# Kernel optimization log

Measured on AMD Instinct MI355X. Metric: run time of the kernel, lower is better.

The kernel has to match this reference:

```python
import jax, jax.numpy as jnp
import numpy as np

H = 512      # hidden_size
GH = 512     # global_hidden_size
V = 128      # VOCAB_SIZE (one-hot arg_hot width)
D = 14       # tree depth; complete binary tree
NUM_OPS = 36
N_INT = 5    # num_internal_ops
N_NODES = 2 ** (D + 1) - 1  # 32767, heap layout: node i has children 2i+1, 2i+2


def _p(key, i, shape, s=0.05):
    return jax.random.normal(jax.random.fold_in(key, i), shape, dtype=jnp.float32) * s


def setup_inputs() -> dict:
    key = jax.random.key(0)
    return {
        "tokens": jax.random.randint(jax.random.fold_in(key, 0), (N_NODES,), 0, V),
        "validity_mask": jnp.ones((NUM_OPS,), jnp.float32),
        # binary tree-LSTM (blstm): 2 children
        "W_iou_b": _p(key, 1, (V, 3 * H)), "U_iou_b": _p(key, 2, (2, H, 3 * H)), "b_iou_b": jnp.zeros((3 * H,), jnp.float32),
        "Wf_b": _p(key, 3, (V, H)), "Uf_b": _p(key, 4, (2, H, H)), "bf_b": jnp.ones((H,), jnp.float32),
        # ternary tree-LSTM (tlstm): 3 children
        "W_iou_t": _p(key, 5, (V, 3 * H)), "U_iou_t": _p(key, 6, (3, H, 3 * H)), "b_iou_t": jnp.zeros((3 * H,), jnp.float32),
        "Wf_t": _p(key, 7, (V, H)), "Uf_t": _p(key, 8, (3, H, H)), "bf_t": jnp.ones((H,), jnp.float32),
        # FFN: one h-by-h layer (ffn_complexity = h^2 * n_layers, n_layers=1)
        "ffn_W": _p(key, 9, (H, H)), "ffn_b": jnp.zeros((H,), jnp.float32),
        # global LSTM (1 layer, 1 step), torch gate order i,f,g,o
        "lstm_Wx": _p(key, 10, (H, 4 * GH)), "lstm_Wh": _p(key, 11, (GH, 4 * GH)), "lstm_b": jnp.zeros((4 * GH,), jnp.float32),
        # actor heads on concat(root_hidden, h_glob)
        "hl_W": _p(key, 12, (H + GH, 2)), "hl_b": jnp.zeros((2,), jnp.float32),
        "int_W": _p(key, 13, (H + GH, N_INT)), "int_b": jnp.zeros((N_INT,), jnp.float32),
        "act_W": _p(key, 14, (H + GH, NUM_OPS)), "act_b": jnp.zeros((NUM_OPS,), jnp.float32),
    }


def _nary_cell(x, hk, ck, W_iou, U_iou, b_iou, Wf, Uf, bf):
    # x: [n, V]; hk, ck: [n, K, H]  (K children)
    iou = x @ W_iou + jnp.einsum('nkh,khg->ng', hk, U_iou) + b_iou
    i, o, u = jnp.split(iou, 3, axis=-1)
    f = jax.nn.sigmoid((x @ Wf + bf)[:, None, :] + jnp.einsum('nkh,khg->nkg', hk, Uf))
    c = jax.nn.sigmoid(i) * jnp.tanh(u) + jnp.sum(f * ck, axis=1)
    h = jax.nn.sigmoid(o) * jnp.tanh(c)
    return h, c


def _forward(tokens, validity_mask, W_iou_b, U_iou_b, b_iou_b, Wf_b, Uf_b, bf_b,
             W_iou_t, U_iou_t, b_iou_t, Wf_t, Uf_t, bf_t, ffn_W, ffn_b,
             lstm_Wx, lstm_Wh, lstm_b, hl_W, hl_b, int_W, int_b, act_W, act_b):
    arg_hot = jax.nn.one_hot(tokens, V, dtype=jnp.float32)  # [N_NODES, V]
    h_prev = c_prev = None
    h_ab = c_ab = None
    # apply_binary_lstm over the whole tree, bottom-up, one batched cell per level
    for lvl in range(D, -1, -1):
        n = 2 ** lvl
        x = arg_hot[n - 1:2 * n - 1]  # level lvl occupies heap slots [2^l-1, 2^{l+1}-2]
        if h_prev is None:
            hk = jnp.zeros((n, 2, H), jnp.float32)  # leaves: tz children
            ck = hk
        else:
            hk = h_prev.reshape(n, 2, H)
            ck = c_prev.reshape(n, 2, H)
        h_prev, c_prev = _nary_cell(x, hk, ck, W_iou_b, U_iou_b, b_iou_b, Wf_b, Uf_b, bf_b)
        if lvl == 1:
            h_ab, c_ab = h_prev, c_prev  # root's children a, b
    # apply_ternary_lstm at depth 0: children = (self.hidden, a.hidden, b.hidden)
    hk3 = jnp.concatenate([h_prev, h_ab], axis=0)[None]  # [1, 3, H]
    ck3 = jnp.concatenate([c_prev, c_ab], axis=0)[None]
    h_root, c_root = _nary_cell(arg_hot[0:1], hk3, ck3, W_iou_t, U_iou_t, b_iou_t, Wf_t, Uf_t, bf_t)
    # apply_ffn (1 layer) then apply_global_lstm (single step from zero state)
    h_f = jnp.maximum(h_root @ ffn_W + ffn_b, 0.0)  # [1, H]
    h_g = jnp.zeros((1, GH), jnp.float32)
    c_g = h_g
    gates = h_f @ lstm_Wx + h_g @ lstm_Wh + lstm_b
    gi, gf, gg, go = jnp.split(gates, 4, axis=-1)
    c_g = jax.nn.sigmoid(gf) * c_g + jax.nn.sigmoid(gi) * jnp.tanh(gg)
    h_g = jax.nn.sigmoid(go) * jnp.tanh(c_g)
    # actor heads
    feat = jnp.concatenate([h_f, h_g], axis=-1)  # [1, H+GH]
    hl = feat @ hl_W + hl_b
    il = feat @ int_W + int_b
    el = jnp.log(validity_mask)[None, :] + feat @ (act_W * validity_mask[None, :]) + act_b * validity_mask
    return jnp.concatenate([hl, il, el], axis=-1)  # [1, 2 + N_INT + NUM_OPS]


def reference(tokens, validity_mask, W_iou_b, U_iou_b, b_iou_b, Wf_b, Uf_b, bf_b,
              W_iou_t, U_iou_t, b_iou_t, Wf_t, Uf_t, bf_t, ffn_W, ffn_b,
              lstm_Wx, lstm_Wh, lstm_b, hl_W, hl_b, int_W, int_b, act_W, act_b):
    return _forward(tokens, validity_mask, W_iou_b, U_iou_b, b_iou_b, Wf_b, Uf_b, bf_b,
                    W_iou_t, U_iou_t, b_iou_t, Wf_t, Uf_t, bf_t, ffn_W, ffn_b,
                    lstm_Wx, lstm_Wh, lstm_b, hl_W, hl_b, int_W, int_b, act_W, act_b)
```

## Files before the change

### kernel.cpp

```cpp
#include <hip/hip_runtime.h>
#include <hip/hip_bf16.h>
#include <math.h>

#define H 512
#define V 128
#define NLEAF 16384

typedef __attribute__((ext_vector_type(4))) float f32x4;
typedef __attribute__((ext_vector_type(8))) short s16x8;
typedef unsigned short ushort_t;

__device__ ushort_t g_hb0[NLEAF * H];
__device__ ushort_t g_hb1[(NLEAF / 2) * H];
__device__ float    g_c0[NLEAF * H];
__device__ float    g_c1[(NLEAF / 2) * H];
__device__ ushort_t g_UiouT[3 * H * 2 * H];
__device__ ushort_t g_UfT[H * 2 * H];
__device__ ushort_t g_UiouTt[3 * H * 3 * H];
__device__ ushort_t g_UfTt[H * 3 * H];
__device__ float    g_rpart[3 * 3072];
__device__ float    g_spart[32 * 2 * 2560];
__device__ float    g_root[2 * H];
__device__ float    g_hf[H];
__device__ float    g_gates[4 * H];

__device__ __forceinline__ float sigm(float x) { return 1.0f / (1.0f + __expf(-x)); }
__device__ __forceinline__ float ftanh(float x) {
  return 1.0f - 2.0f / (__expf(2.0f * x) + 1.0f);
}
__device__ __forceinline__ ushort_t f2bf(float x) {
  __hip_bfloat16 b = __float2bfloat16(x);
  return *reinterpret_cast<ushort_t*>(&b);
}
__device__ __forceinline__ float bf2f(ushort_t u) {
  union { unsigned int i; float f; } v; v.i = ((unsigned int)u) << 16; return v.f;
}
__device__ __forceinline__ void gload_lds16(const void* g, void* l) {
  __builtin_amdgcn_global_load_lds(
      (const __attribute__((address_space(1))) unsigned int*)g,
      (__attribute__((address_space(3))) unsigned int*)l, 16, 0, 0);
}

__global__ __launch_bounds__(256) void k_transp(const float* __restrict__ src,
                                                ushort_t* __restrict__ dst,
                                                int R, int Cc) {
  __shared__ float t[32][33];
  int bc = blockIdx.x * 32, br = blockIdx.y * 32;
  int tx = threadIdx.x & 31, ty = threadIdx.x >> 5;
  for (int rr = ty; rr < 32; rr += 8)
    t[rr][tx] = src[(size_t)(br + rr) * Cc + bc + tx];
  __syncthreads();
  for (int rr = ty; rr < 32; rr += 8)
    dst[(size_t)(bc + rr) * R + br + tx] = f2bf(t[tx][rr]);
}

__global__ __launch_bounds__(256) void k_leaf(const int* __restrict__ tokens,
                                              const float* __restrict__ Wiou,
                                              const float* __restrict__ biou) {
  int idx = blockIdx.x * 256 + threadIdx.x;
  int i = idx >> 9, j = idx & (H - 1);
  int tok = tokens[(NLEAF - 1) + i];
  const float* Wr = Wiou + (size_t)tok * 3 * H;
  float ig = Wr[j] + biou[j];
  float og = Wr[H + j] + biou[H + j];
  float ug = Wr[2 * H + j] + biou[2 * H + j];
  float c = sigm(ig) * ftanh(ug);
  float h = sigm(og) * ftanh(c);
  g_hb0[idx] = f2bf(h);
  g_c0[idx] = c;
}

__global__ __launch_bounds__(256, 2) void k_mfma_lvl(int lvl,
    const int* __restrict__ tokens,
    const float* __restrict__ Wiou, const float* __restrict__ biou,
    const float* __restrict__ Wf, const float* __restrict__ bf) {
  const int n = 1 << lvl;
  const int node0 = n - 1;
  const int outp = lvl & 1;
  const ushort_t* __restrict__ hprev = outp ? g_hb0 : g_hb1;
  const float* __restrict__ cprev = outp ? g_c0 : g_c1;
  ushort_t* __restrict__ hout = outp ? g_hb1 : g_hb0;
  float* __restrict__ cout = outp ? g_c1 : g_c0;

  const int i0 = blockIdx.x * 128;
  const int j0 = blockIdx.y * 64;
  const int tid = threadIdx.x;
  const int lane = tid & 63;
  const int w = tid >> 6;
  const int wry = w >> 1;
  const int cx = w & 1;

  __shared__ f32x4 smemv[3072];
  char* smem = (char*)smemv;

  const char* gp[6];
  unsigned lb[6], lstride[6];
  {
    int kb = (lane >> 4) * 16;
    #pragma unroll
    for (int q = 0; q < 6; ++q) {
      int c = w * 6 + q;
      if (c < 8) {
        int row = i0 + c * 16 + (lane & 15);
        gp[q] = (const char*)hprev + (size_t)row * 2048 + kb;
        lb[q] = c * 1024u;
        lstride[q] = 8192u;
      } else {
        int ct = c - 8;
        int col = ct * 16 + (lane & 15);
        int g = col >> 6, jj = j0 + (col & 63);
        const ushort_t* Ub = (g < 3) ? (g_UiouT + (size_t)(g * 512 + jj) * 1024)
                                     : (g_UfT + (size_t)jj * 1024);
        gp[q] = (const char*)Ub + kb;
        lb[q] = 16384u + ct * 1024u;
        lstride[q] = 16384u;
      }
    }
  }

#define STAGE(BUF)                                                   \
  {                                                                  \
    _Pragma("unroll")                                                \
    for (int q = 0; q < 6; ++q) {                                    \
      gload_lds16(gp[q], smem + lb[q] + (unsigned)(BUF) * lstride[q]); \
      gp[q] += 64;                                                   \
    }                                                                \
  }

  f32x4 acc[4][10];
  #pragma unroll
  for (int a = 0; a < 4; ++a)
    #pragma unroll
    for (int b = 0; b < 10; ++b) acc[a][b] = (f32x4){0.f, 0.f, 0.f, 0.f};

#define COMPUTE(FA)                                                          \
  {                                                                          \
    const char* ab = smem + buf * 8192 + wry * 4096 + lane * 16;             \
    s16x8 a0 = *(const s16x8*)(ab);                                          \
    s16x8 a1 = *(const s16x8*)(ab + 1024);                                   \
    s16x8 a2 = *(const s16x8*)(ab + 2048);                                   \
    s16x8 a3 = *(const s16x8*)(ab + 3072);                                   \
    const char* bb = smem + 16384 + buf * 16384 + cx * 2048 + lane * 16;     \
    s16x8 b0 = *(const s16x8*)(bb);                                          \
    s16x8 b1 = *(const s16x8*)(bb + 1024);                                   \
    s16x8 b2 = *(const s16x8*)(bb + 4096);                                   \
    s16x8 b3 = *(const s16x8*)(bb + 5120);                                   \
    s16x8 b4 = *(const s16x8*)(bb + 8192);                                   \
    s16x8 b5 = *(const s16x8*)(bb + 9216);                                   \
    s16x8 b6 = *(const s16x8*)(bb + 12288);                                  \
    s16x8 b7 = *(const s16x8*)(bb + 13312);                                  \
    s16x8 aa[4] = {a0, a1, a2, a3};                                          \
    _Pragma("unroll")                                                        \
    for (int rtl = 0; rtl < 4; ++rtl) {                                      \
      acc[rtl][0] = __builtin_amdgcn_mfma_f32_16x16x32_bf16(aa[rtl], b0, acc[rtl][0], 0, 0, 0); \
      acc[rtl][1] = __builtin_amdgcn_mfma_f32_16x16x32_bf16(aa[rtl], b1, acc[rtl][1], 0, 0, 0); \
      acc[rtl][2] = __builtin_amdgcn_mfma_f32_16x16x32_bf16(aa[rtl], b2, acc[rtl][2], 0, 0, 0); \
      acc[rtl][3] = __builtin_amdgcn_mfma_f32_16x16x32_bf16(aa[rtl], b3, acc[rtl][3], 0, 0, 0); \
      acc[rtl][4] = __builtin_amdgcn_mfma_f32_16x16x32_bf16(aa[rtl], b4, acc[rtl][4], 0, 0, 0); \
      acc[rtl][5] = __builtin_amdgcn_mfma_f32_16x16x32_bf16(aa[rtl], b5, acc[rtl][5], 0, 0, 0); \
      acc[rtl][FA] = __builtin_amdgcn_mfma_f32_16x16x32_bf16(aa[rtl], b6, acc[rtl][FA], 0, 0, 0); \
      acc[rtl][FA + 1] = __builtin_amdgcn_mfma_f32_16x16x32_bf16(aa[rtl], b7, acc[rtl][FA + 1], 0, 0, 0); \
    }                                                                        \
  }

  STAGE(0);
  __syncthreads();
  int buf = 0;
  for (int kt = 0; kt < 16; ++kt) {
    STAGE(buf ^ 1);
    COMPUTE(6);
    __syncthreads();
    buf ^= 1;
  }
  for (int kt = 16; kt < 32; ++kt) {
    if (kt < 31) STAGE(buf ^ 1);
    COMPUTE(8);
    __syncthreads();
    buf ^= 1;
  }
#undef COMPUTE
#undef STAGE

  const int node_c = lane >> 4;
  const int jl = lane & 15;
  #pragma unroll
  for (int t = 0; t < 2; ++t) {
    const int j = j0 + cx * 32 + t * 16 + jl;
    const float bi = biou[j], bo = biou[512 + j], bu = biou[1024 + j], bfv = bf[j];
    #pragma unroll
    for (int rtl = 0; rtl < 4; ++rtl) {
      f32x4 vi = acc[rtl][0 + t], vo = acc[rtl][2 + t], vu = acc[rtl][4 + t],
            v0 = acc[rtl][6 + t], v1 = acc[rtl][8 + t];
      const int ib = i0 + wry * 64 + rtl * 16 + node_c * 4;
      #pragma unroll
      for (int r = 0; r < 4; ++r) {
        int i = ib + r;
        if (i < n) {
          int tok = tokens[node0 + i];
          const float* Wr = Wiou + (size_t)tok * 1536;
          float fpre = Wf[(size_t)tok * 512 + j] + bfv;
          float ig = vi[r] + Wr[j] + bi;
          float og = vo[r] + Wr[512 + j] + bo;
          float ug = vu[r] + Wr[1024 + j] + bu;
          float cc = sigm(ig) * ftanh(ug)
                   + sigm(fpre + v0[r]) * cprev[(size_t)(2 * i) * 512 + j]
                   + sigm(fpre + v1[r]) * cprev[(size_t)(2 * i + 1) * 512 + j];
          float hh = sigm(og) * ftanh(cc);
          hout[(size_t)i * 512 + j] = f2bf(hh);
          cout[(size_t)i * 512 + j] = cc;
        }
      }
    }
  }
}

__global__ __launch_bounds__(256) void k_sm_p1(int lvl) {
  const int outp = lvl & 1;
  const ushort_t* __restrict__ hprev = outp ? g_hb0 : g_hb1;
  const int i = blockIdx.z;
  const int by = blockIdx.y;
  const int tid = threadIdx.x;
  const int c = blockIdx.x * 256 + tid;

  __shared__ float hl[512];
  hl[tid] = bf2f(hprev[(size_t)i * 1024 + by * 512 + tid]);
  hl[256 + tid] = bf2f(hprev[(size_t)i * 1024 + by * 512 + 256 + tid]);
  __syncthreads();

  float acc = 0.f;
  const ushort_t* col = nullptr;
  if (c < 1536) {
    col = g_UiouT + (size_t)c * 1024 + by * 512;
  } else {
    int v = c - 1536;
    if ((v >> 9) == by) col = g_UfT + (size_t)(v & 511) * 1024 + by * 512;
  }
  if (col) {
    #pragma unroll 4
    for (int k0 = 0; k0 < 512; k0 += 8) {
      s16x8 wv = *(const s16x8*)(col + k0);
      #pragma unroll
      for (int r = 0; r < 8; ++r) acc += hl[k0 + r] * bf2f((ushort_t)wv[r]);
    }
  }
  g_spart[((size_t)i * 2 + by) * 2560 + c] = acc;
}

__global__ __launch_bounds__(512) void k_sm_p2(int lvl,
    const int* __restrict__ tokens,
    const float* __restrict__ Wiou, const float* __restrict__ biou,
    const float* __restrict__ Wf, const float* __restrict__ bf) {
  const int n = 1 << lvl;
  const int node0 = n - 1;
  const int outp = lvl & 1;
  const float* __restrict__ cprev = outp ? g_c0 : g_c1;
  ushort_t* __restrict__ hout = outp ? g_hb1 : g_hb0;
  float* __restrict__ cout = outp ? g_c1 : g_c0;

  const int i = blockIdx.x;
  const int j = threadIdx.x;
  const float* sp = g_spart + (size_t)i * 2 * 2560;

  float ai = sp[j] + sp[2560 + j];
  float ao = sp[512 + j] + sp[2560 + 512 + j];
  float au = sp[1024 + j] + sp[2560 + 1024 + j];
  float af0 = sp[1536 + j] + sp[2560 + 1536 + j];
  float af1 = sp[2048 + j] + sp[2560 + 2048 + j];

  int tok = tokens[node0 + i];
  const float* Wr = Wiou + (size_t)tok * 1536;
  float fpre = Wf[(size_t)tok * 512 + j] + bf[j];
  float ig = ai + Wr[j] + biou[j];
  float og = ao + Wr[512 + j] + biou[512 + j];
  float ug = au + Wr[1024 + j] + biou[1024 + j];
  float cc = sigm(ig) * ftanh(ug)
           + sigm(fpre + af0) * cprev[(size_t)(2 * i) * 512 + j]
           + sigm(fpre + af1) * cprev[(size_t)(2 * i + 1) * 512 + j];
  float hh = sigm(og) * ftanh(cc);
  hout[(size_t)i * 512 + j] = f2bf(hh);
  cout[(size_t)i * 512 + j] = cc;
}

__global__ __launch_bounds__(256) void k_root_p1() {
  const int by = blockIdx.y;
  const int tid = threadIdx.x;
  const int c = blockIdx.x * 256 + tid;

  __shared__ float hl[512];
  {
    int m0 = by * 512;
    #pragma unroll
    for (int q = 0; q < 2; ++q) {
      int t = tid + q * 256, m = m0 + t;
      hl[t] = (m < 512) ? bf2f(g_hb0[m]) : bf2f(g_hb1[m - 512]);
    }
  }
  __syncthreads();

  float acc = 0.f;
  const ushort_t* col = nullptr;
  if (c < 1536) {
    col = g_UiouTt + (size_t)c * 1536 + by * 512;
  } else {
    int v = c - 1536;
    if ((v >> 9) == by) col = g_UfTt + (size_t)(v & 511) * 1536 + by * 512;
  }
  if (col) {
    #pragma unroll 4
    for (int k0 = 0; k0 < 512; k0 += 8) {
      s16x8 wv = *(const s16x8*)(col + k0);
      #pragma unroll
      for (int r = 0; r < 8; ++r) acc += hl[k0 + r] * bf2f((ushort_t)wv[r]);
    }
  }
  g_rpart[(size_t)by * 3072 + c] = acc;
}

__global__ __launch_bounds__(512) void k_root_p2(const int* __restrict__ tokens,
    const float* __restrict__ Wiou_t, const float* __restrict__ biou_t,
    const float* __restrict__ Wf_t, const float* __restrict__ bf_t) {
  const int j = threadIdx.x;
  float ai = g_rpart[j] + g_rpart[3072 + j] + g_rpart[6144 + j];
  float ao = g_rpart[512 + j] + g_rpart[3072 + 512 + j] + g_rpart[6144 + 512 + j];
  float au = g_rpart[1024 + j] + g_rpart[3072 + 1024 + j] + g_rpart[6144 + 1024 + j];
  float f0 = g_rpart[1536 + j] + g_rpart[3072 + 1536 + j] + g_rpart[6144 + 1536 + j];
  float f1 = g_rpart[2048 + j] + g_rpart[3072 + 2048 + j] + g_rpart[6144 + 2048 + j];
  float f2 = g_rpart[2560 + j] + g_rpart[3072 + 2560 + j] + g_rpart[6144 + 2560 + j];

  int tok = tokens[0];
  float fpre = Wf_t[(size_t)tok * H + j] + bf_t[j];
  float ig = ai + Wiou_t[(size_t)tok * 3 * H + j] + biou_t[j];
  float og = ao + Wiou_t[(size_t)tok * 3 * H + H + j] + biou_t[H + j];
  float ug = au + Wiou_t[(size_t)tok * 3 * H + 2 * H + j] + biou_t[2 * H + j];
  float cc = sigm(ig) * ftanh(ug)
           + sigm(fpre + f0) * g_c0[j]
           + sigm(fpre + f1) * g_c1[j]
           + sigm(fpre + f2) * g_c1[H + j];
  float hh = sigm(og) * ftanh(cc);
  g_root[j] = hh;
  g_root[H + j] = cc;
}

__global__ __launch_bounds__(512) void k_head1(const float* __restrict__ ffnW,
                                               const float* __restrict__ ffnb) {
  __shared__ float hr[H];
  int j = threadIdx.x;
  hr[j] = g_root[j];
  __syncthreads();
  float acc = ffnb[j];
  #pragma unroll 8
  for (int m = 0; m < H; ++m) acc += hr[m] * ffnW[m * H + j];
  g_hf[j] = fmaxf(acc, 0.0f);
}

__global__ __launch_bounds__(64) void k_head2(const float* __restrict__ Wx,
                                              const float* __restrict__ lb) {
  int g = blockIdx.x * 64 + threadIdx.x;
  float acc = lb[g];
  #pragma unroll 8
  for (int m = 0; m < H; ++m) acc += g_hf[m] * Wx[m * 4 * H + g];
  g_gates[g] = acc;
}

__global__ __launch_bounds__(512) void k_head3(const float* __restrict__ vm,
    const float* __restrict__ hlW, const float* __restrict__ hlb,
    const float* __restrict__ intW, const float* __restrict__ intb,
    const float* __restrict__ actW, const float* __restrict__ actb,
    float* __restrict__ out) {
  __shared__ float feat[2 * H];
  int j = threadIdx.x;
  float ci = sigm(g_gates[j]) * ftanh(g_gates[2 * H + j]);
  float hg = sigm(g_gates[3 * H + j]) * ftanh(ci);
  feat[j] = g_hf[j];
  feat[H + j] = hg;
  __syncthreads();

  const int wv = threadIdx.x >> 6;
  const int lane = threadIdx.x & 63;
  for (int o = wv; o < 43; o += 8) {
    const float* Wc;
    int stride, colb;
    if (o < 2)       { Wc = hlW;  stride = 2;  colb = o; }
    else if (o < 7)  { Wc = intW; stride = 5;  colb = o - 2; }
    else             { Wc = actW; stride = 36; colb = o - 7; }
    float s = 0.f;
    #pragma unroll
    for (int q = 0; q < 16; ++q) {
      int m = lane + q * 64;
      s += feat[m] * Wc[(size_t)m * stride + colb];
    }
    #pragma unroll
    for (int d = 32; d >= 1; d >>= 1) s += __shfl_xor(s, d);
    if (lane == 0) {
      float res;
      if (o < 2)      res = s + hlb[o];
      else if (o < 7) res = s + intb[o - 2];
      else {
        int a = o - 7;
        float v = vm[a];
        res = __logf(v) + s * v + actb[a] * v;
      }
      out[o] = res;
    }
  }
}

extern "C" void kernel_launch(void* const* d_in, const int* in_sizes, int n_in,
                              void* d_out, int out_size, void* d_ws, size_t ws_size,
                              hipStream_t stream) {
  (void)in_sizes; (void)n_in; (void)d_ws; (void)ws_size; (void)out_size;
  const int* tokens   = (const int*)d_in[0];
  const float* vm     = (const float*)d_in[1];
  const float* Wiou_b = (const float*)d_in[2];
  const float* Uiou_b = (const float*)d_in[3];
  const float* biou_b = (const float*)d_in[4];
  const float* Wf_b   = (const float*)d_in[5];
  const float* Uf_b   = (const float*)d_in[6];
  const float* bf_b   = (const float*)d_in[7];
  const float* Wiou_t = (const float*)d_in[8];
  const float* Uiou_t = (const float*)d_in[9];
  const float* biou_t = (const float*)d_in[10];
  const float* Wf_t   = (const float*)d_in[11];
  const float* Uf_t   = (const float*)d_in[12];
  const float* bf_t   = (const float*)d_in[13];
  const float* ffnW   = (const float*)d_in[14];
  const float* ffnb   = (const float*)d_in[15];
  const float* lstmWx = (const float*)d_in[16];
  const float* lstmb  = (const float*)d_in[18];
  const float* hlW    = (const float*)d_in[19];
  const float* hlb    = (const float*)d_in[20];
  const float* intW   = (const float*)d_in[21];
  const float* intb   = (const float*)d_in[22];
  const float* actW   = (const float*)d_in[23];
  const float* actb   = (const float*)d_in[24];

  ushort_t* UiouT;  hipGetSymbolAddress((void**)&UiouT, HIP_SYMBOL(g_UiouT));
  ushort_t* UfT;    hipGetSymbolAddress((void**)&UfT, HIP_SYMBOL(g_UfT));
  ushort_t* UiouTt; hipGetSymbolAddress((void**)&UiouTt, HIP_SYMBOL(g_UiouTt));
  ushort_t* UfTt;   hipGetSymbolAddress((void**)&UfTt, HIP_SYMBOL(g_UfTt));

  k_transp<<<dim3(48, 32), 256, 0, stream>>>(Uiou_b, UiouT, 1024, 1536);
  k_transp<<<dim3(16, 32), 256, 0, stream>>>(Uf_b, UfT, 1024, 512);
  k_transp<<<dim3(48, 48), 256, 0, stream>>>(Uiou_t, UiouTt, 1536, 1536);
  k_transp<<<dim3(16, 48), 256, 0, stream>>>(Uf_t, UfTt, 1536, 512);

  k_leaf<<<NLEAF * H / 256, 256, 0, stream>>>(tokens, Wiou_b, biou_b);
  for (int lvl = 13; lvl >= 6; --lvl) {
    int gx = (1 << lvl) / 128; if (gx < 1) gx = 1;
    k_mfma_lvl<<<dim3(gx, 8), 256, 0, stream>>>(lvl, tokens, Wiou_b, biou_b,
                                                Wf_b, bf_b);
  }
  for (int lvl = 5; lvl >= 0; --lvl) {
    int n = 1 << lvl;
    k_sm_p1<<<dim3(10, 2, n), 256, 0, stream>>>(lvl);
    k_sm_p2<<<n, 512, 0, stream>>>(lvl, tokens, Wiou_b, biou_b, Wf_b, bf_b);
  }
  k_root_p1<<<dim3(12, 3), 256, 0, stream>>>();
  k_root_p2<<<1, 512, 0, stream>>>(tokens, Wiou_t, biou_t, Wf_t, bf_t);
  k_head1<<<1, 512, 0, stream>>>(ffnW, ffnb);
  k_head2<<<32, 64, 0, stream>>>(lstmWx, lstmb);
  k_head3<<<1, 512, 0, stream>>>(vm, hlW, hlb, intW, intb, actW, actb, (float*)d_out);
}
```

Before: 671.9 us.

## Shrink MFMA level tiles, vectorize leaf kernel, fuse small-level GEMV passes

The MFMA level kernel drops from 128-row tiles with 4 waves to 64-row tiles with 2 waves, each wave covering all 64 rows and 32 columns. This doubles block count on the mid-size levels to fill more CUs, at the cost of less B-tile reuse per block. The leaf kernel becomes a grid-stride loop with float4 loads and vector stores. The two-kernel small-level path (partial sums plus combine) is merged into one kernel that reduces in shared memory, removing a launch and the global partial buffer per level.

```diff
diff --git a/kernel.cpp b/kernel.cpp
--- a/kernel.cpp
+++ b/kernel.cpp
@@ -8,6 +8,7 @@
 
 typedef __attribute__((ext_vector_type(4))) float f32x4;
 typedef __attribute__((ext_vector_type(8))) short s16x8;
+typedef __attribute__((ext_vector_type(4))) unsigned short u16x4;
 typedef unsigned short ushort_t;
 
 __device__ ushort_t g_hb0[NLEAF * H];
@@ -19,7 +20,6 @@
 __device__ ushort_t g_UiouTt[3 * H * 3 * H];
 __device__ ushort_t g_UfTt[H * 3 * H];
 __device__ float    g_rpart[3 * 3072];
-__device__ float    g_spart[32 * 2 * 2560];
 __device__ float    g_root[2 * H];
 __device__ float    g_hf[H];
 __device__ float    g_gates[4 * H];
@@ -57,20 +57,29 @@
 __global__ __launch_bounds__(256) void k_leaf(const int* __restrict__ tokens,
                                               const float* __restrict__ Wiou,
                                               const float* __restrict__ biou) {
-  int idx = blockIdx.x * 256 + threadIdx.x;
-  int i = idx >> 9, j = idx & (H - 1);
-  int tok = tokens[(NLEAF - 1) + i];
-  const float* Wr = Wiou + (size_t)tok * 3 * H;
-  float ig = Wr[j] + biou[j];
-  float og = Wr[H + j] + biou[H + j];
-  float ug = Wr[2 * H + j] + biou[2 * H + j];
-  float c = sigm(ig) * ftanh(ug);
-  float h = sigm(og) * ftanh(c);
-  g_hb0[idx] = f2bf(h);
-  g_c0[idx] = c;
-}
-
-__global__ __launch_bounds__(256, 2) void k_mfma_lvl(int lvl,
+  const int total = NLEAF * 128;
+  for (int q = blockIdx.x * 256 + threadIdx.x; q < total; q += gridDim.x * 256) {
+    int i = q >> 7, jv = q & 127;
+    int tok = tokens[(NLEAF - 1) + i];
+    const f32x4* Wr = (const f32x4*)(Wiou + (size_t)tok * 1536);
+    const f32x4* bv = (const f32x4*)biou;
+    f32x4 wi = Wr[jv] + bv[jv];
+    f32x4 wo = Wr[128 + jv] + bv[128 + jv];
+    f32x4 wu = Wr[256 + jv] + bv[256 + jv];
+    u16x4 hv; f32x4 cv;
+    #pragma unroll
+    for (int r = 0; r < 4; ++r) {
+      float c = sigm(wi[r]) * ftanh(wu[r]);
+      float h = sigm(wo[r]) * ftanh(c);
+      cv[r] = c;
+      hv[r] = f2bf(h);
+    }
+    *reinterpret_cast<u16x4*>(&g_hb0[(size_t)q * 4]) = hv;
+    *reinterpret_cast<f32x4*>(&g_c0[(size_t)q * 4]) = cv;
+  }
+}
+
+__global__ __launch_bounds__(128, 2) void k_mfma_lvl(int lvl,
     const int* __restrict__ tokens,
     const float* __restrict__ Wiou, const float* __restrict__ biou,
     const float* __restrict__ Wf, const float* __restrict__ bf) {
@@ -82,49 +91,47 @@
   ushort_t* __restrict__ hout = outp ? g_hb1 : g_hb0;
   float* __restrict__ cout = outp ? g_c1 : g_c0;
 
-  const int i0 = blockIdx.x * 128;
+  const int i0 = blockIdx.x * 64;
   const int j0 = blockIdx.y * 64;
   const int tid = threadIdx.x;
   const int lane = tid & 63;
   const int w = tid >> 6;
-  const int wry = w >> 1;
-  const int cx = w & 1;
-
-  __shared__ f32x4 smemv[3072];
+
+  __shared__ f32x4 smemv[2560];
   char* smem = (char*)smemv;
 
-  const char* gp[6];
-  unsigned lb[6], lstride[6];
+  const char* gp[10];
+  unsigned lb[10], lstr[10];
   {
     int kb = (lane >> 4) * 16;
     #pragma unroll
-    for (int q = 0; q < 6; ++q) {
-      int c = w * 6 + q;
-      if (c < 8) {
+    for (int q = 0; q < 10; ++q) {
+      int c = w * 10 + q;
+      if (c < 4) {
         int row = i0 + c * 16 + (lane & 15);
         gp[q] = (const char*)hprev + (size_t)row * 2048 + kb;
         lb[q] = c * 1024u;
-        lstride[q] = 8192u;
+        lstr[q] = 4096u;
       } else {
-        int ct = c - 8;
+        int ct = c - 4;
         int col = ct * 16 + (lane & 15);
         int g = col >> 6, jj = j0 + (col & 63);
         const ushort_t* Ub = (g < 3) ? (g_UiouT + (size_t)(g * 512 + jj) * 1024)
                                      : (g_UfT + (size_t)jj * 1024);
         gp[q] = (const char*)Ub + kb;
-        lb[q] = 16384u + ct * 1024u;
-        lstride[q] = 16384u;
+        lb[q] = 8192u + ct * 1024u;
+        lstr[q] = 16384u;
       }
     }
   }
 
-#define STAGE(BUF)                                                   \
-  {                                                                  \
-    _Pragma("unroll")                                                \
-    for (int q = 0; q < 6; ++q) {                                    \
-      gload_lds16(gp[q], smem + lb[q] + (unsigned)(BUF) * lstride[q]); \
-      gp[q] += 64;                                                   \
-    }                                                                \
+#define STAGE(BUF)                                                     \
+  {                                                                    \
+    _Pragma("unroll")                                                  \
+    for (int q = 0; q < 10; ++q) {                                     \
+      gload_lds16(gp[q], smem + lb[q] + (unsigned)(BUF) * lstr[q]);    \
+      gp[q] += 64;                                                     \
+    }                                                                  \
   }
 
   f32x4 acc[4][10];
@@ -135,12 +142,12 @@
 
 #define COMPUTE(FA)                                                          \
   {                                                                          \
-    const char* ab = smem + buf * 8192 + wry * 4096 + lane * 16;             \
+    const char* ab = smem + buf * 4096 + lane * 16;                          \
     s16x8 a0 = *(const s16x8*)(ab);                                          \
     s16x8 a1 = *(const s16x8*)(ab + 1024);                                   \
     s16x8 a2 = *(const s16x8*)(ab + 2048);                                   \
     s16x8 a3 = *(const s16x8*)(ab + 3072);                                   \
-    const char* bb = smem + 16384 + buf * 16384 + cx * 2048 + lane * 16;     \
+    const char* bb = smem + 8192 + buf * 16384 + w * 2048 + lane * 16;       \
     s16x8 b0 = *(const s16x8*)(bb);                                          \
     s16x8 b1 = *(const s16x8*)(bb + 1024);                                   \
     s16x8 b2 = *(const s16x8*)(bb + 4096);                                   \
@@ -185,100 +192,93 @@
   const int jl = lane & 15;
   #pragma unroll
   for (int t = 0; t < 2; ++t) {
-    const int j = j0 + cx * 32 + t * 16 + jl;
+    const int j = j0 + w * 32 + t * 16 + jl;
     const float bi = biou[j], bo = biou[512 + j], bu = biou[1024 + j], bfv = bf[j];
     #pragma unroll
     for (int rtl = 0; rtl < 4; ++rtl) {
       f32x4 vi = acc[rtl][0 + t], vo = acc[rtl][2 + t], vu = acc[rtl][4 + t],
             v0 = acc[rtl][6 + t], v1 = acc[rtl][8 + t];
-      const int ib = i0 + wry * 64 + rtl * 16 + node_c * 4;
+      const int ib = i0 + rtl * 16 + node_c * 4;
       #pragma unroll
       for (int r = 0; r < 4; ++r) {
         int i = ib + r;
-        if (i < n) {
-          int tok = tokens[node0 + i];
-          const float* Wr = Wiou + (size_t)tok * 1536;
-          float fpre = Wf[(size_t)tok * 512 + j] + bfv;
-          float ig = vi[r] + Wr[j] + bi;
-          float og = vo[r] + Wr[512 + j] + bo;
-          float ug = vu[r] + Wr[1024 + j] + bu;
-          float cc = sigm(ig) * ftanh(ug)
-                   + sigm(fpre + v0[r]) * cprev[(size_t)(2 * i) * 512 + j]
-                   + sigm(fpre + v1[r]) * cprev[(size_t)(2 * i + 1) * 512 + j];
-          float hh = sigm(og) * ftanh(cc);
-          hout[(size_t)i * 512 + j] = f2bf(hh);
-          cout[(size_t)i * 512 + j] = cc;
-        }
+        int tok = tokens[node0 + i];
+        const float* Wr = Wiou + (size_t)tok * 1536;
+        float fpre = Wf[(size_t)tok * 512 + j] + bfv;
+        float ig = vi[r] + Wr[j] + bi;
+        float og = vo[r] + Wr[512 + j] + bo;
+        float ug = vu[r] + Wr[1024 + j] + bu;
+        float cc = sigm(ig) * ftanh(ug)
+                 + sigm(fpre + v0[r]) * cprev[(size_t)(2 * i) * 512 + j]
+                 + sigm(fpre + v1[r]) * cprev[(size_t)(2 * i + 1) * 512 + j];
+        float hh = sigm(og) * ftanh(cc);
+        hout[(size_t)i * 512 + j] = f2bf(hh);
+        cout[(size_t)i * 512 + j] = cc;
       }
     }
   }
 }
 
-__global__ __launch_bounds__(256) void k_sm_p1(int lvl) {
-  const int outp = lvl & 1;
-  const ushort_t* __restrict__ hprev = outp ? g_hb0 : g_hb1;
-  const int i = blockIdx.z;
-  const int by = blockIdx.y;
-  const int tid = threadIdx.x;
-  const int c = blockIdx.x * 256 + tid;
-
-  __shared__ float hl[512];
-  hl[tid] = bf2f(hprev[(size_t)i * 1024 + by * 512 + tid]);
-  hl[256 + tid] = bf2f(hprev[(size_t)i * 1024 + by * 512 + 256 + tid]);
-  __syncthreads();
-
-  float acc = 0.f;
-  const ushort_t* col = nullptr;
-  if (c < 1536) {
-    col = g_UiouT + (size_t)c * 1024 + by * 512;
-  } else {
-    int v = c - 1536;
-    if ((v >> 9) == by) col = g_UfT + (size_t)(v & 511) * 1024 + by * 512;
-  }
-  if (col) {
-    #pragma unroll 4
-    for (int k0 = 0; k0 < 512; k0 += 8) {
-      s16x8 wv = *(const s16x8*)(col + k0);
-      #pragma unroll
-      for (int r = 0; r < 8; ++r) acc += hl[k0 + r] * bf2f((ushort_t)wv[r]);
-    }
-  }
-  g_spart[((size_t)i * 2 + by) * 2560 + c] = acc;
-}
-
-__global__ __launch_bounds__(512) void k_sm_p2(int lvl,
+__global__ __launch_bounds__(256) void k_small(int lvl,
     const int* __restrict__ tokens,
     const float* __restrict__ Wiou, const float* __restrict__ biou,
     const float* __restrict__ Wf, const float* __restrict__ bf) {
   const int n = 1 << lvl;
   const int node0 = n - 1;
   const int outp = lvl & 1;
+  const ushort_t* __restrict__ hprev = outp ? g_hb0 : g_hb1;
   const float* __restrict__ cprev = outp ? g_c0 : g_c1;
   ushort_t* __restrict__ hout = outp ? g_hb1 : g_hb0;
   float* __restrict__ cout = outp ? g_c1 : g_c0;
 
-  const int i = blockIdx.x;
-  const int j = threadIdx.x;
-  const float* sp = g_spart + (size_t)i * 2 * 2560;
-
-  float ai = sp[j] + sp[2560 + j];
-  float ao = sp[512 + j] + sp[2560 + 512 + j];
-  float au = sp[1024 + j] + sp[2560 + 1024 + j];
-  float af0 = sp[1536 + j] + sp[2560 + 1536 + j];
-  float af1 = sp[2048 + j] + sp[2560 + 2048 + j];
-
-  int tok = tokens[node0 + i];
-  const float* Wr = Wiou + (size_t)tok * 1536;
-  float fpre = Wf[(size_t)tok * 512 + j] + bf[j];
-  float ig = ai + Wr[j] + biou[j];
-  float og = ao + Wr[512 + j] + biou[512 + j];
-  float ug = au + Wr[1024 + j] + biou[1024 + j];
-  float cc = sigm(ig) * ftanh(ug)
-           + sigm(fpre + af0) * cprev[(size_t)(2 * i) * 512 + j]
-           + sigm(fpre + af1) * cprev[(size_t)(2 * i + 1) * 512 + j];
-  float hh = sigm(og) * ftanh(cc);
-  hout[(size_t)i * 512 + j] = f2bf(hh);
-  cout[(size_t)i * 512 + j] = cc;
+  const int i = blockIdx.y;
+  const int j0 = blockIdx.x * 64;
+  const int tid = threadIdx.x;
+  const int g = tid >> 6;
+  const int jc = tid & 63;
+  const int jj = j0 + jc;
+
+  __shared__ float hl[1024];
+  __shared__ float exch[5][64];
+  for (int t = tid; t < 1024; t += 256) hl[t] = bf2f(hprev[(size_t)i * 1024 + t]);
+  __syncthreads();
+
+  const ushort_t* col = (g < 3) ? (g_UiouT + (size_t)(g * 512 + jj) * 1024)
+                                : (g_UfT + (size_t)jj * 1024);
+  float a0 = 0.f, a1 = 0.f;
+  #pragma unroll 4
+  for (int k0 = 0; k0 < 512; k0 += 8) {
+    s16x8 wv = *(const s16x8*)(col + k0);
+    #pragma unroll
+    for (int r = 0; r < 8; ++r) a0 += hl[k0 + r] * bf2f((ushort_t)wv[r]);
+  }
+  #pragma unroll 4
+  for (int k0 = 512; k0 < 1024; k0 += 8) {
+    s16x8 wv = *(const s16x8*)(col + k0);
+    #pragma unroll
+    for (int r = 0; r < 8; ++r) a1 += hl[k0 + r] * bf2f((ushort_t)wv[r]);
+  }
+  if (g < 3) exch[g][jc] = a0 + a1;
+  else { exch[3][jc] = a0; exch[4][jc] = a1; }
+  __syncthreads();
+
+  if (tid < 64) {
+    int j = j0 + tid;
+    float ai = exch[0][tid], ao = exch[1][tid], au = exch[2][tid];
+    float af0 = exch[3][tid], af1 = exch[4][tid];
+    int tok = tokens[node0 + i];
+    const float* Wr = Wiou + (size_t)tok * 1536;
+    float fpre = Wf[(size_t)tok * 512 + j] + bf[j];
+    float ig = ai + Wr[j] + biou[j];
+    float og = ao + Wr[512 + j] + biou[512 + j];
+    float ug = au + Wr[1024 + j] + biou[1024 + j];
+    float cc = sigm(ig) * ftanh(ug)
+             + sigm(fpre + af0) * cprev[(size_t)(2 * i) * 512 + j]
+             + sigm(fpre + af1) * cprev[(size_t)(2 * i + 1) * 512 + j];
+    float hh = sigm(og) * ftanh(cc);
+    hout[(size_t)i * 512 + j] = f2bf(hh);
+    cout[(size_t)i * 512 + j] = cc;
+  }
 }
 
 __global__ __launch_bounds__(256) void k_root_p1() {
@@ -444,16 +444,16 @@
   k_transp<<<dim3(48, 48), 256, 0, stream>>>(Uiou_t, UiouTt, 1536, 1536);
   k_transp<<<dim3(16, 48), 256, 0, stream>>>(Uf_t, UfTt, 1536, 512);
 
-  k_leaf<<<NLEAF * H / 256, 256, 0, stream>>>(tokens, Wiou_b, biou_b);
+  k_leaf<<<2048, 256, 0, stream>>>(tokens, Wiou_b, biou_b);
   for (int lvl = 13; lvl >= 6; --lvl) {
-    int gx = (1 << lvl) / 128; if (gx < 1) gx = 1;
-    k_mfma_lvl<<<dim3(gx, 8), 256, 0, stream>>>(lvl, tokens, Wiou_b, biou_b,
+    int gx = (1 << lvl) / 64;
+    k_mfma_lvl<<<dim3(gx, 8), 128, 0, stream>>>(lvl, tokens, Wiou_b, biou_b,
                                                 Wf_b, bf_b);
   }
   for (int lvl = 5; lvl >= 0; --lvl) {
     int n = 1 << lvl;
-    k_sm_p1<<<dim3(10, 2, n), 256, 0, stream>>>(lvl);
-    k_sm_p2<<<n, 512, 0, stream>>>(lvl, tokens, Wiou_b, biou_b, Wf_b, bf_b);
+    k_small<<<dim3(8, n), 256, 0, stream>>>(lvl, tokens, Wiou_b, biou_b,
+                                            Wf_b, bf_b);
   }
   k_root_p1<<<dim3(12, 3), 256, 0, stream>>>();
   k_root_p2<<<1, 512, 0, stream>>>(tokens, Wiou_t, biou_t, Wf_t, bf_t);
```

Result: faster. 654.2 us (-2.6%).
